# Kernel tuning notes

Measured on AMD Instinct MI355X. Metric: run time of the kernel, lower is better.

The kernel has to match this reference:

```python
import jax, jax.numpy as jnp
import numpy as np

K = 4          # conv kernel size
DIL = 3        # conv dilation
EPS = 1e-5     # rms eps inside gate kernel
NORM_EPS = 1e-5  # RMSNorm eps for value rms


def setup_inputs() -> dict:
    key = jax.random.key(0)
    ks = jax.random.split(key, 10)
    B, T, G, C, E = 2, 4096, 4, 1024, 1024
    return {
        "embeddings": jax.random.normal(ks[0], (B, T, E), jnp.float32),
        "hidden_states": jax.random.normal(ks[1], (B, T, G, C), jnp.float32),
        "key_w": jax.random.normal(ks[2], (G * C, E), jnp.float32) * 0.02,
        "key_b": jax.random.normal(ks[3], (G * C,), jnp.float32) * 0.02,
        "value_w": jax.random.normal(ks[4], (C, E), jnp.float32) * 0.02,
        "value_b": jax.random.normal(ks[5], (C,), jnp.float32) * 0.02,
        "w_key_norm": jax.random.uniform(ks[6], (G, C), jnp.float32, 0.5, 1.5),
        "w_query_norm": jax.random.uniform(ks[7], (G, C), jnp.float32, 0.5, 1.5),
        "w_norm": jax.random.uniform(ks[8], (G, C), jnp.float32, 0.5, 1.5),
        "conv_weight": jax.random.normal(ks[9], (G * C, K), jnp.float32) * 0.1,
    }


def reference(embeddings, hidden_states, key_w, key_b, value_w, value_b,
              w_key_norm, w_query_norm, w_norm, conv_weight):
    B, T, G, C = hidden_states.shape
    # projections
    k_all = (embeddings @ key_w.T + key_b).reshape(B, T, G, C)     # [B,T,G,C]
    q_all = hidden_states                                          # [B,T,G,C]
    vproj = embeddings @ value_w.T + value_b                       # [B,T,C]

    # gate kernel: per (b,t,g) RMS of key/query + weighted dot -> sign-sqrt-sigmoid gate
    rms_k = jnp.sqrt(jnp.mean(k_all * k_all, axis=-1) + EPS)       # [B,T,G]
    rms_q = jnp.sqrt(jnp.mean(q_all * q_all, axis=-1) + EPS)       # [B,T,G]
    dot = jnp.einsum('btgc,gc,btgc,gc->btg', k_all, w_key_norm, q_all, w_query_norm)
    gate_raw = dot / (rms_k * rms_q) / jnp.sqrt(jnp.float32(C))
    gate = jax.nn.sigmoid(jnp.where(gate_raw >= 0, 1.0, -1.0)
                          * jnp.sqrt(jnp.maximum(jnp.abs(gate_raw), 1e-6)))
    value = vproj[:, :, None, :] * gate[..., None]                 # [B,T,G,C]
    rms_v = jnp.sqrt(jnp.mean(value * value, axis=-1) + NORM_EPS)  # [B,T,G]

    # conv+residual kernel: per-group RMS-norm, dilated depthwise causal conv, SiLU, residual
    normed = value * (w_norm[None, None] / rms_v[..., None])       # [B,T,G,C]
    conv_w = conv_weight.reshape(G, C, K)                          # depthwise weights
    pad = (K - 1) * DIL
    xp = jnp.pad(normed, ((0, 0), (pad, 0), (0, 0), (0, 0)))
    # acc[b,t,g,c] = sum_k normed[b, t-(K-1-k)*DIL, g, c] * conv_w[g,c,k]
    acc = xp[:, 0:T] * conv_w[None, None, :, :, 0]
    for k in range(1, K):
        acc = acc + xp[:, k * DIL: k * DIL + T] * conv_w[None, None, :, :, k]
    acc = acc * jax.nn.sigmoid(acc)  # SiLU activation
    return value + acc
```

## Files before the change

kernel.cpp:

```cpp
#include <hip/hip_runtime.h>
#include <hip/hip_bf16.h>
#include <cstdint>
#include <cstddef>

using bf16 = __hip_bfloat16;

typedef __bf16 bf16x8_t __attribute__((ext_vector_type(8)));
typedef float  f32x4_t  __attribute__((ext_vector_type(4)));

static constexpr int Bb = 2;
static constexpr int Tt = 4096;
static constexpr int Gg = 4;
static constexpr int Cc = 1024;
static constexpr int Mm = Bb * Tt;
static constexpr int GC = Gg * Cc;

__device__ __forceinline__ float bfbits2f(unsigned u) {
  union { unsigned i; float f; } c; c.i = u << 16; return c.f;
}
__device__ __forceinline__ ushort f2bfbits(float v) {
  union { __hip_bfloat16 h; ushort u; } c; c.h = __float2bfloat16(v); return c.u;
}

__device__ __forceinline__ void store_val(bf16* p, float v)  { *p = __float2bfloat16(v); }
__device__ __forceinline__ void store_val(float* p, float v) { *p = v; }

__device__ __forceinline__ void gld_lds16(const ushort* g, ushort* l) {
  __builtin_amdgcn_global_load_lds(
      (const __attribute__((address_space(1))) void*)g,
      (__attribute__((address_space(3))) void*)l, 16, 0, 0);
}

__global__ __launch_bounds__(256)
void cvt_bf16(const float* __restrict__ in, ushort* __restrict__ out, int n4)
{
  const int i = blockIdx.x * 256 + threadIdx.x;
  if (i >= n4) return;
  const float4 v = ((const float4*)in)[i];
  ushort4 o;
  o.x = f2bfbits(v.x); o.y = f2bfbits(v.y);
  o.z = f2bfbits(v.z); o.w = f2bfbits(v.w);
  ((ushort4*)out)[i] = o;
}

__global__ __launch_bounds__(256)
void cvt_split(const float* __restrict__ in, ushort* __restrict__ hi,
               ushort* __restrict__ lo, int n4)
{
  const int i = blockIdx.x * 256 + threadIdx.x;
  if (i >= n4) return;
  const float4 v = ((const float4*)in)[i];
  ushort4 h, l;
  h.x = f2bfbits(v.x); l.x = f2bfbits(v.x - bfbits2f(h.x));
  h.y = f2bfbits(v.y); l.y = f2bfbits(v.y - bfbits2f(h.y));
  h.z = f2bfbits(v.z); l.z = f2bfbits(v.z - bfbits2f(h.z));
  h.w = f2bfbits(v.w); l.w = f2bfbits(v.w - bfbits2f(h.w));
  ((ushort4*)hi)[i] = h;
  ((ushort4*)lo)[i] = l;
}

__global__ __launch_bounds__(256, 2)
void gemm_key_fused(const ushort* __restrict__ embH, const ushort* __restrict__ embL,
                    const ushort* __restrict__ kwH,  const ushort* __restrict__ kwL,
                    const float* __restrict__ key_b, const float* __restrict__ hid,
                    const float* __restrict__ wkn,   const float* __restrict__ wqn,
                    float* __restrict__ k2_part, float* __restrict__ dot_part,
                    float* __restrict__ q2_part)
{
  constexpr int K = Cc;
  __shared__ __align__(16) ushort sAH[128 * 64];
  __shared__ __align__(16) ushort sAL[128 * 64];
  __shared__ __align__(16) ushort sBH[128 * 64];
  __shared__ __align__(16) ushort sBL[128 * 64];

  const int tid  = threadIdx.x;
  const int lane = tid & 63;
  const int wave = tid >> 6;
  const int wm   = wave & 1;
  const int wn   = wave >> 1;
  const int row0 = blockIdx.y * 128;
  const int col0 = blockIdx.x * 128;

  const int srow = tid >> 3;
  const int scol = ((tid & 7) ^ (srow & 7)) * 8;
  const int wofs = wave * 512;

  f32x4_t acc[4][4] = {};

  for (int kt = 0; kt < K; kt += 64) {
#pragma unroll
    for (int p = 0; p < 4; ++p) {
      const size_t aoff = (size_t)(row0 + p * 32 + srow) * K + kt + scol;
      const size_t boff = (size_t)(col0 + p * 32 + srow) * K + kt + scol;
      gld_lds16(embH + aoff, sAH + p * 2048 + wofs);
      gld_lds16(embL + aoff, sAL + p * 2048 + wofs);
      gld_lds16(kwH  + boff, sBH + p * 2048 + wofs);
      gld_lds16(kwL  + boff, sBL + p * 2048 + wofs);
    }
    __syncthreads();

#pragma unroll
    for (int ks = 0; ks < 2; ++ks) {
      const int cb = ks * 4 + (lane >> 4);
      const int ce = ((cb ^ (lane & 7)) * 8);
      bf16x8_t afH[4], afL[4], bfH[4], bfL[4];
#pragma unroll
      for (int mi = 0; mi < 4; ++mi) {
        const int r = wm * 64 + mi * 16 + (lane & 15);
        afH[mi] = *(const bf16x8_t*)(sAH + r * 64 + ce);
        afL[mi] = *(const bf16x8_t*)(sAL + r * 64 + ce);
      }
#pragma unroll
      for (int ni = 0; ni < 4; ++ni) {
        const int r = wn * 64 + ni * 16 + (lane & 15);
        bfH[ni] = *(const bf16x8_t*)(sBH + r * 64 + ce);
        bfL[ni] = *(const bf16x8_t*)(sBL + r * 64 + ce);
      }
#pragma unroll
      for (int mi = 0; mi < 4; ++mi)
#pragma unroll
        for (int ni = 0; ni < 4; ++ni) {
          acc[mi][ni] = __builtin_amdgcn_mfma_f32_16x16x32_bf16(
              afH[mi], bfH[ni], acc[mi][ni], 0, 0, 0);
          acc[mi][ni] = __builtin_amdgcn_mfma_f32_16x16x32_bf16(
              afH[mi], bfL[ni], acc[mi][ni], 0, 0, 0);
          acc[mi][ni] = __builtin_amdgcn_mfma_f32_16x16x32_bf16(
              afL[mi], bfH[ni], acc[mi][ni], 0, 0, 0);
        }
    }
    __syncthreads();
  }

  const int lrow = lane >> 4;
  const int lcol = lane & 15;
  const int g    = col0 >> 10;

  float s2[4][4] = {};
  float su[4][4] = {};
  float sq[4][4] = {};

#pragma unroll
  for (int ni = 0; ni < 4; ++ni) {
    const int col = col0 + wn * 64 + ni * 16 + lcol;
    const float kb = key_b[col];
    const float ww = wkn[col] * wqn[col];
#pragma unroll
    for (int mi = 0; mi < 4; ++mi) {
      const int rowb = row0 + wm * 64 + mi * 16 + lrow * 4;
#pragma unroll
      for (int r = 0; r < 4; ++r) {
        const float q = hid[(size_t)(rowb + r) * GC + col];
        const float k = acc[mi][ni][r] + kb;
        s2[mi][r] += k * k;
        su[mi][r] += k * ww * q;
        sq[mi][r] += q * q;
      }
    }
  }
#pragma unroll
  for (int off = 1; off < 16; off <<= 1) {
#pragma unroll
    for (int mi = 0; mi < 4; ++mi)
#pragma unroll
      for (int r = 0; r < 4; ++r) {
        s2[mi][r] += __shfl_xor(s2[mi][r], off);
        su[mi][r] += __shfl_xor(su[mi][r], off);
        sq[mi][r] += __shfl_xor(sq[mi][r], off);
      }
  }
  if (lcol == 0) {
#pragma unroll
    for (int mi = 0; mi < 4; ++mi) {
      const int rowb = row0 + wm * 64 + mi * 16 + lrow * 4;
#pragma unroll
      for (int r = 0; r < 4; ++r) {
        atomicAdd(&k2_part[(rowb + r) * Gg + g],  s2[mi][r]);
        atomicAdd(&dot_part[(rowb + r) * Gg + g], su[mi][r]);
        atomicAdd(&q2_part[(rowb + r) * Gg + g],  sq[mi][r]);
      }
    }
  }
}

template <typename OutT>
__global__ __launch_bounds__(256, 2)
void gemm_bt(const ushort* __restrict__ A, const ushort* __restrict__ Bm,
             const float* __restrict__ bias, OutT* __restrict__ C,
             int M, int N, int K)
{
  __shared__ __align__(16) ushort sA[128 * 64];
  __shared__ __align__(16) ushort sB[128 * 64];

  const int tid  = threadIdx.x;
  const int lane = tid & 63;
  const int wave = tid >> 6;
  const int wm   = wave & 1;
  const int wn   = wave >> 1;
  const int row0 = blockIdx.y * 128;
  const int col0 = blockIdx.x * 128;

  const int srow = tid >> 3;
  const int scol = ((tid & 7) ^ (srow & 7)) * 8;
  ushort* aWB = sA + wave * 512;
  ushort* bWB = sB + wave * 512;

  f32x4_t acc[4][4] = {};

  for (int kt = 0; kt < K; kt += 64) {
#pragma unroll
    for (int p = 0; p < 4; ++p) {
      gld_lds16(A  + (size_t)(row0 + p * 32 + srow) * K + kt + scol,
                aWB + p * 2048);
      gld_lds16(Bm + (size_t)(col0 + p * 32 + srow) * K + kt + scol,
                bWB + p * 2048);
    }
    __syncthreads();

#pragma unroll
    for (int ks = 0; ks < 2; ++ks) {
      const int cb = ks * 4 + (lane >> 4);
      const int ce = ((cb ^ (lane & 7)) * 8);
      bf16x8_t af[4], bfr[4];
#pragma unroll
      for (int mi = 0; mi < 4; ++mi) {
        const int r = wm * 64 + mi * 16 + (lane & 15);
        af[mi] = *(const bf16x8_t*)(sA + r * 64 + ce);
      }
#pragma unroll
      for (int ni = 0; ni < 4; ++ni) {
        const int r = wn * 64 + ni * 16 + (lane & 15);
        bfr[ni] = *(const bf16x8_t*)(sB + r * 64 + ce);
      }
#pragma unroll
      for (int mi = 0; mi < 4; ++mi)
#pragma unroll
        for (int ni = 0; ni < 4; ++ni)
          acc[mi][ni] = __builtin_amdgcn_mfma_f32_16x16x32_bf16(
              af[mi], bfr[ni], acc[mi][ni], 0, 0, 0);
    }
    __syncthreads();
  }

  const int lrow = lane >> 4;
  const int lcol = lane & 15;
#pragma unroll
  for (int ni = 0; ni < 4; ++ni) {
    const int col = col0 + wn * 64 + ni * 16 + lcol;
    const float bv = bias[col];
#pragma unroll
    for (int mi = 0; mi < 4; ++mi) {
      const int rowb = row0 + wm * 64 + mi * 16 + lrow * 4;
#pragma unroll
      for (int r = 0; r < 4; ++r)
        store_val(&C[(size_t)(rowb + r) * N + col], acc[mi][ni][r] + bv);
    }
  }
}

__global__ __launch_bounds__(256)
void finalize_kernel(const float* __restrict__ vproj,
                     const float* __restrict__ k2_part,
                     const float* __restrict__ dot_part,
                     const float* __restrict__ q2_part,
                     float* __restrict__ gate_o, float* __restrict__ snorm_o)
{
  const int bt   = blockIdx.x;
  const int tid  = threadIdx.x;
  const int g    = tid >> 6;
  const int lane = tid & 63;

  const float4 v4 = ((const float4*)(vproj + (size_t)bt * Cc))[tid];
  float pv = v4.x * v4.x + v4.y * v4.y + v4.z * v4.z + v4.w * v4.w;
#pragma unroll
  for (int off = 32; off > 0; off >>= 1) pv += __shfl_xor(pv, off);
  __shared__ float wsum[4];
  if (lane == 0) wsum[g] = pv;
  __syncthreads();

  if (lane == 0) {
    const float mv = (wsum[0] + wsum[1] + wsum[2] + wsum[3]) * (1.0f / 1024.0f);
    const float sk = k2_part[bt * Gg + g];
    const float sd = dot_part[bt * Gg + g];
    const float sq = q2_part[bt * Gg + g];
    const float rk = sqrtf(sk * (1.0f / 1024.0f) + 1e-5f);
    const float rq = sqrtf(sq * (1.0f / 1024.0f) + 1e-5f);
    const float graw = sd / (rk * rq) * (1.0f / 32.0f);
    const float sgn = (graw >= 0.f) ? 1.f : -1.f;
    const float gate = 1.f / (1.f + expf(-sgn * sqrtf(fmaxf(fabsf(graw), 1e-6f))));
    const float rv = sqrtf(gate * gate * mv + 1e-5f);
    gate_o[bt * Gg + g]  = gate;
    snorm_o[bt * Gg + g] = gate / rv;
  }
}

static constexpr int CJ  = 128;
static constexpr int NCH = 11;

__global__ __launch_bounds__(256)
void conv_kernel(const float* __restrict__ vproj, const float* __restrict__ gate,
                 const float* __restrict__ snorm, const float* __restrict__ wnm,
                 const float* __restrict__ cw, float* __restrict__ out)
{
  int x = blockIdx.x;
  const int cb = x & 3;  x >>= 2;
  const int p  = x % 3;  x /= 3;
  const int ch = x % NCH; x /= NCH;
  const int g  = x & 3;  x >>= 2;
  const int b  = x;
  const int c  = cb * 256 + threadIdx.x;

  const float wn = wnm[g * Cc + c];
  const float4 w = ((const float4*)cw)[g * Cc + c];

  int t = p + 3 * (ch * CJ);
  if (t >= Tt) return;

  float n1 = 0.f, n2 = 0.f, n3 = 0.f;
#pragma unroll
  for (int h = 3; h >= 1; --h) {
    const int th = t - 3 * h;
    float nv = 0.f;
    if (th >= 0) {
      const int bt = b * Tt + th;
      nv = vproj[(size_t)bt * Cc + c] * snorm[bt * Gg + g] * wn;
    }
    n3 = n2; n2 = n1; n1 = nv;
  }

  for (int j = 0; j < CJ && t < Tt; ++j, t += 3) {
    const int bt = b * Tt + t;
    const float vp  = vproj[(size_t)bt * Cc + c];
    const float gt  = gate[bt * Gg + g];
    const float sn  = snorm[bt * Gg + g];
    const float cur = vp * sn * wn;
    const float a   = w.x * n3 + w.y * n2 + w.z * n1 + w.w * cur;
    const float si  = a / (1.f + __expf(-a));
    out[((size_t)bt * Gg + g) * Cc + c] = vp * gt + si;
    n3 = n2; n2 = n1; n1 = cur;
  }
}

extern "C" void kernel_launch(void* const* d_in, const int* in_sizes, int n_in,
                              void* d_out, int out_size, void* d_ws, size_t ws_size,
                              hipStream_t stream)
{
  const float* emb   = (const float*)d_in[0];
  const float* hid   = (const float*)d_in[1];
  const float* key_w = (const float*)d_in[2];
  const float* key_b = (const float*)d_in[3];
  const float* val_w = (const float*)d_in[4];
  const float* val_b = (const float*)d_in[5];
  const float* wkn   = (const float*)d_in[6];
  const float* wqn   = (const float*)d_in[7];
  const float* wnm   = (const float*)d_in[8];
  const float* cwt   = (const float*)d_in[9];
  float* out = (float*)d_out;

  char* ws = (char*)d_ws;
  ushort* embH  = (ushort*)ws;  ws += (size_t)Mm * Cc * 2;
  ushort* embL  = (ushort*)ws;  ws += (size_t)Mm * Cc * 2;
  ushort* kwH   = (ushort*)ws;  ws += (size_t)GC * Cc * 2;
  ushort* kwL   = (ushort*)ws;  ws += (size_t)GC * Cc * 2;
  ushort* vwB   = (ushort*)ws;  ws += (size_t)Cc * Cc * 2;
  float*  vproj = (float*)ws;   ws += (size_t)Mm * Cc * 4;
  float*  k2p   = (float*)ws;   ws += (size_t)Mm * Gg * 4;
  float*  dotp  = (float*)ws;   ws += (size_t)Mm * Gg * 4;
  float*  q2p   = (float*)ws;   ws += (size_t)Mm * Gg * 4;
  float*  gate  = (float*)ws;   ws += (size_t)Mm * Gg * 4;
  float*  snorm = (float*)ws;

  hipMemsetAsync(k2p, 0, (size_t)3 * Mm * Gg * 4, stream);

  dim3 blk(256);
  cvt_split<<<dim3((Mm * Cc / 4) / 256), blk, 0, stream>>>(emb,   embH, embL, Mm * Cc / 4);
  cvt_split<<<dim3((GC * Cc / 4) / 256), blk, 0, stream>>>(key_w, kwH,  kwL,  GC * Cc / 4);
  cvt_bf16 <<<dim3((Cc * Cc / 4) / 256), blk, 0, stream>>>(val_w, vwB,  Cc * Cc / 4);

  gemm_key_fused<<<dim3(GC / 128, Mm / 128), blk, 0, stream>>>(
      embH, embL, kwH, kwL, key_b, hid, wkn, wqn, k2p, dotp, q2p);

  gemm_bt<float><<<dim3(Cc / 128, Mm / 128), blk, 0, stream>>>(
      embH, vwB, val_b, vproj, Mm, Cc, Cc);

  finalize_kernel<<<dim3(Mm), blk, 0, stream>>>(vproj, k2p, dotp, q2p, gate, snorm);

  const int nblocks = Bb * Gg * NCH * 3 * (Cc / 256);
  conv_kernel<<<dim3(nblocks), blk, 0, stream>>>(vproj, gate, snorm, wnm, cwt, out);
}
```

Before: 600.6 us.

## Double-buffer LDS tiles in both GEMM kernels to overlap loads with MFMA

Both the fused key GEMM and the generic bf16 GEMM now use two LDS buffers and prefetch the next K-tile with direct global-to-LDS loads while the current tile feeds the MFMAs. Explicit vmcnt waits and raw barriers replace __syncthreads. The split-bf16 key kernel also shrinks its K-tile from 64 to 32 with a new XOR swizzle, so the LDS footprint stays the same as before. The aim is to hide global memory latency behind compute, at the cost of more barriers per K step in the key kernel and reliance on hand-counted vmcnt values.

```diff
diff --git a/kernel.cpp b/kernel.cpp
--- a/kernel.cpp
+++ b/kernel.cpp
@@ -67,11 +67,12 @@
                     float* __restrict__ k2_part, float* __restrict__ dot_part,
                     float* __restrict__ q2_part)
 {
-  constexpr int K = Cc;
-  __shared__ __align__(16) ushort sAH[128 * 64];
-  __shared__ __align__(16) ushort sAL[128 * 64];
-  __shared__ __align__(16) ushort sBH[128 * 64];
-  __shared__ __align__(16) ushort sBL[128 * 64];
+  constexpr int K  = Cc;
+  constexpr int NT = K / 32;
+  __shared__ __align__(16) ushort sAH[2 * 4096];
+  __shared__ __align__(16) ushort sAL[2 * 4096];
+  __shared__ __align__(16) ushort sBH[2 * 4096];
+  __shared__ __align__(16) ushort sBL[2 * 4096];
 
   const int tid  = threadIdx.x;
   const int lane = tid & 63;
@@ -81,54 +82,81 @@
   const int row0 = blockIdx.y * 128;
   const int col0 = blockIdx.x * 128;
 
-  const int srow = tid >> 3;
-  const int scol = ((tid & 7) ^ (srow & 7)) * 8;
+  const int sr0 = tid >> 2;
+  const int sch = tid & 3;
   const int wofs = wave * 512;
 
+  int gcol[2]; int grA[2];
+#pragma unroll
+  for (int p = 0; p < 2; ++p) {
+    const int r = p * 64 + sr0;
+    gcol[p] = ((sch ^ ((r + (r >> 2)) & 3)) * 8);
+    grA[p]  = r;
+  }
+
   f32x4_t acc[4][4] = {};
 
-  for (int kt = 0; kt < K; kt += 64) {
-#pragma unroll
-    for (int p = 0; p < 4; ++p) {
-      const size_t aoff = (size_t)(row0 + p * 32 + srow) * K + kt + scol;
-      const size_t boff = (size_t)(col0 + p * 32 + srow) * K + kt + scol;
-      gld_lds16(embH + aoff, sAH + p * 2048 + wofs);
-      gld_lds16(embL + aoff, sAL + p * 2048 + wofs);
-      gld_lds16(kwH  + boff, sBH + p * 2048 + wofs);
-      gld_lds16(kwL  + boff, sBL + p * 2048 + wofs);
-    }
-    __syncthreads();
-
-#pragma unroll
-    for (int ks = 0; ks < 2; ++ks) {
-      const int cb = ks * 4 + (lane >> 4);
-      const int ce = ((cb ^ (lane & 7)) * 8);
-      bf16x8_t afH[4], afL[4], bfH[4], bfL[4];
-#pragma unroll
-      for (int mi = 0; mi < 4; ++mi) {
-        const int r = wm * 64 + mi * 16 + (lane & 15);
-        afH[mi] = *(const bf16x8_t*)(sAH + r * 64 + ce);
-        afL[mi] = *(const bf16x8_t*)(sAL + r * 64 + ce);
-      }
+  auto stage = [&](int kt, int b) {
+    const int kk = kt * 32;
+#pragma unroll
+    for (int p = 0; p < 2; ++p) {
+      const size_t ao = (size_t)(row0 + grA[p]) * K + kk + gcol[p];
+      const size_t bo = (size_t)(col0 + grA[p]) * K + kk + gcol[p];
+      const int d = b * 4096 + p * 2048 + wofs;
+      gld_lds16(embH + ao, sAH + d);
+      gld_lds16(embL + ao, sAL + d);
+      gld_lds16(kwH  + bo, sBH + d);
+      gld_lds16(kwL  + bo, sBL + d);
+    }
+  };
+
+  stage(0, 0);
+  int cur = 0;
+
+  for (int kt = 0; kt < NT; ++kt) {
+    if (kt + 1 < NT) {
+      stage(kt + 1, cur ^ 1);
+      asm volatile("s_waitcnt vmcnt(8)" ::: "memory");
+    } else {
+      asm volatile("s_waitcnt vmcnt(0)" ::: "memory");
+    }
+    asm volatile("s_barrier" ::: "memory");
+
+    const ushort* bAH = sAH + cur * 4096;
+    const ushort* bAL = sAL + cur * 4096;
+    const ushort* bBH = sBH + cur * 4096;
+    const ushort* bBL = sBL + cur * 4096;
+    const int ch = lane >> 4;
+
+    bf16x8_t afH[4], afL[4], bfH[4], bfL[4];
+#pragma unroll
+    for (int mi = 0; mi < 4; ++mi) {
+      const int r  = wm * 64 + mi * 16 + (lane & 15);
+      const int co = ((ch ^ ((r + (r >> 2)) & 3)) * 8);
+      afH[mi] = *(const bf16x8_t*)(bAH + r * 32 + co);
+      afL[mi] = *(const bf16x8_t*)(bAL + r * 32 + co);
+    }
+#pragma unroll
+    for (int ni = 0; ni < 4; ++ni) {
+      const int r  = wn * 64 + ni * 16 + (lane & 15);
+      const int co = ((ch ^ ((r + (r >> 2)) & 3)) * 8);
+      bfH[ni] = *(const bf16x8_t*)(bBH + r * 32 + co);
+      bfL[ni] = *(const bf16x8_t*)(bBL + r * 32 + co);
+    }
+#pragma unroll
+    for (int mi = 0; mi < 4; ++mi)
 #pragma unroll
       for (int ni = 0; ni < 4; ++ni) {
-        const int r = wn * 64 + ni * 16 + (lane & 15);
-        bfH[ni] = *(const bf16x8_t*)(sBH + r * 64 + ce);
-        bfL[ni] = *(const bf16x8_t*)(sBL + r * 64 + ce);
-      }
-#pragma unroll
-      for (int mi = 0; mi < 4; ++mi)
-#pragma unroll
-        for (int ni = 0; ni < 4; ++ni) {
-          acc[mi][ni] = __builtin_amdgcn_mfma_f32_16x16x32_bf16(
-              afH[mi], bfH[ni], acc[mi][ni], 0, 0, 0);
-          acc[mi][ni] = __builtin_amdgcn_mfma_f32_16x16x32_bf16(
-              afH[mi], bfL[ni], acc[mi][ni], 0, 0, 0);
-          acc[mi][ni] = __builtin_amdgcn_mfma_f32_16x16x32_bf16(
-              afL[mi], bfH[ni], acc[mi][ni], 0, 0, 0);
-        }
-    }
-    __syncthreads();
+        acc[mi][ni] = __builtin_amdgcn_mfma_f32_16x16x32_bf16(
+            afH[mi], bfH[ni], acc[mi][ni], 0, 0, 0);
+        acc[mi][ni] = __builtin_amdgcn_mfma_f32_16x16x32_bf16(
+            afH[mi], bfL[ni], acc[mi][ni], 0, 0, 0);
+        acc[mi][ni] = __builtin_amdgcn_mfma_f32_16x16x32_bf16(
+            afL[mi], bfH[ni], acc[mi][ni], 0, 0, 0);
+      }
+
+    asm volatile("s_barrier" ::: "memory");
+    cur ^= 1;
   }
 
   const int lrow = lane >> 4;
@@ -188,8 +216,8 @@
              const float* __restrict__ bias, OutT* __restrict__ C,
              int M, int N, int K)
 {
-  __shared__ __align__(16) ushort sA[128 * 64];
-  __shared__ __align__(16) ushort sB[128 * 64];
+  __shared__ __align__(16) ushort sA[2 * 128 * 64];
+  __shared__ __align__(16) ushort sB[2 * 128 * 64];
 
   const int tid  = threadIdx.x;
   const int lane = tid & 63;
@@ -201,20 +229,36 @@
 
   const int srow = tid >> 3;
   const int scol = ((tid & 7) ^ (srow & 7)) * 8;
-  ushort* aWB = sA + wave * 512;
-  ushort* bWB = sB + wave * 512;
+  const int wofs = wave * 512;
 
   f32x4_t acc[4][4] = {};
 
-  for (int kt = 0; kt < K; kt += 64) {
+  const int NT = K / 64;
+
+  auto stage = [&](int kt, int b) {
+    const int kk = kt * 64;
 #pragma unroll
     for (int p = 0; p < 4; ++p) {
-      gld_lds16(A  + (size_t)(row0 + p * 32 + srow) * K + kt + scol,
-                aWB + p * 2048);
-      gld_lds16(Bm + (size_t)(col0 + p * 32 + srow) * K + kt + scol,
-                bWB + p * 2048);
-    }
-    __syncthreads();
+      const int d = b * 8192 + p * 2048 + wofs;
+      gld_lds16(A  + (size_t)(row0 + p * 32 + srow) * K + kk + scol, sA + d);
+      gld_lds16(Bm + (size_t)(col0 + p * 32 + srow) * K + kk + scol, sB + d);
+    }
+  };
+
+  stage(0, 0);
+  int cur = 0;
+
+  for (int kt = 0; kt < NT; ++kt) {
+    if (kt + 1 < NT) {
+      stage(kt + 1, cur ^ 1);
+      asm volatile("s_waitcnt vmcnt(8)" ::: "memory");
+    } else {
+      asm volatile("s_waitcnt vmcnt(0)" ::: "memory");
+    }
+    asm volatile("s_barrier" ::: "memory");
+
+    const ushort* bA = sA + cur * 8192;
+    const ushort* bB = sB + cur * 8192;
 
 #pragma unroll
     for (int ks = 0; ks < 2; ++ks) {
@@ -224,12 +268,12 @@
 #pragma unroll
       for (int mi = 0; mi < 4; ++mi) {
         const int r = wm * 64 + mi * 16 + (lane & 15);
-        af[mi] = *(const bf16x8_t*)(sA + r * 64 + ce);
+        af[mi] = *(const bf16x8_t*)(bA + r * 64 + ce);
       }
 #pragma unroll
       for (int ni = 0; ni < 4; ++ni) {
         const int r = wn * 64 + ni * 16 + (lane & 15);
-        bfr[ni] = *(const bf16x8_t*)(sB + r * 64 + ce);
+        bfr[ni] = *(const bf16x8_t*)(bB + r * 64 + ce);
       }
 #pragma unroll
       for (int mi = 0; mi < 4; ++mi)
@@ -238,7 +282,9 @@
           acc[mi][ni] = __builtin_amdgcn_mfma_f32_16x16x32_bf16(
               af[mi], bfr[ni], acc[mi][ni], 0, 0, 0);
     }
-    __syncthreads();
+
+    asm volatile("s_barrier" ::: "memory");
+    cur ^= 1;
   }
 
   const int lrow = lane >> 4;
```

Measured after the change: 633.4 us. 5.5% more time.

## Halve key GEMM LDS footprint by interleaving hi/lo in one tile, raise occupancy

Applied to the files above, without the earlier changes.

The fused key GEMM now packs the hi and lo bf16 halves of each 32-wide K slice into a single 64-column swizzled LDS tile per operand, which halves its shared memory use from 64KB to 32KB. The K step drops from 64 to 32, so there are twice as many iterations and barriers. Launch bounds for both GEMM kernels go from 2 to 4 blocks per SM, which may force register limits and spills given the 16 accumulator fragments. The goal is more resident waves to hide global-to-LDS latency, at the cost of more sync overhead per unit of work.

```diff
diff --git a/kernel.cpp b/kernel.cpp
--- a/kernel.cpp
+++ b/kernel.cpp
@@ -59,7 +59,7 @@
   ((ushort4*)lo)[i] = l;
 }
 
-__global__ __launch_bounds__(256, 2)
+__global__ __launch_bounds__(256, 4)
 void gemm_key_fused(const ushort* __restrict__ embH, const ushort* __restrict__ embL,
                     const ushort* __restrict__ kwH,  const ushort* __restrict__ kwL,
                     const float* __restrict__ key_b, const float* __restrict__ hid,
@@ -68,10 +68,8 @@
                     float* __restrict__ q2_part)
 {
   constexpr int K = Cc;
-  __shared__ __align__(16) ushort sAH[128 * 64];
-  __shared__ __align__(16) ushort sAL[128 * 64];
-  __shared__ __align__(16) ushort sBH[128 * 64];
-  __shared__ __align__(16) ushort sBL[128 * 64];
+  __shared__ __align__(16) ushort sA[128 * 64];
+  __shared__ __align__(16) ushort sB[128 * 64];
 
   const int tid  = threadIdx.x;
   const int lane = tid & 63;
@@ -82,52 +80,51 @@
   const int col0 = blockIdx.x * 128;
 
   const int srow = tid >> 3;
-  const int scol = ((tid & 7) ^ (srow & 7)) * 8;
-  const int wofs = wave * 512;
+  const int schk = (tid & 7) ^ (srow & 7);
+  const ushort* aBase = (schk < 4) ? embH : embL;
+  const ushort* bBase = (schk < 4) ? kwH  : kwL;
+  const int selem = (schk & 3) * 8;
+  const int wofs  = wave * 512;
 
   f32x4_t acc[4][4] = {};
 
-  for (int kt = 0; kt < K; kt += 64) {
+  for (int kt = 0; kt < K; kt += 32) {
 #pragma unroll
     for (int p = 0; p < 4; ++p) {
-      const size_t aoff = (size_t)(row0 + p * 32 + srow) * K + kt + scol;
-      const size_t boff = (size_t)(col0 + p * 32 + srow) * K + kt + scol;
-      gld_lds16(embH + aoff, sAH + p * 2048 + wofs);
-      gld_lds16(embL + aoff, sAL + p * 2048 + wofs);
-      gld_lds16(kwH  + boff, sBH + p * 2048 + wofs);
-      gld_lds16(kwL  + boff, sBL + p * 2048 + wofs);
+      gld_lds16(aBase + (size_t)(row0 + p * 32 + srow) * K + kt + selem,
+                sA + p * 2048 + wofs);
+      gld_lds16(bBase + (size_t)(col0 + p * 32 + srow) * K + kt + selem,
+                sB + p * 2048 + wofs);
     }
     __syncthreads();
 
-#pragma unroll
-    for (int ks = 0; ks < 2; ++ks) {
-      const int cb = ks * 4 + (lane >> 4);
-      const int ce = ((cb ^ (lane & 7)) * 8);
-      bf16x8_t afH[4], afL[4], bfH[4], bfL[4];
-#pragma unroll
-      for (int mi = 0; mi < 4; ++mi) {
-        const int r = wm * 64 + mi * 16 + (lane & 15);
-        afH[mi] = *(const bf16x8_t*)(sAH + r * 64 + ce);
-        afL[mi] = *(const bf16x8_t*)(sAL + r * 64 + ce);
-      }
+    const int cH = (lane >> 4) ^ (lane & 7);
+    const int cL = cH ^ 4;
+
+    bf16x8_t afH[4], afL[4], bfH[4], bfL[4];
+#pragma unroll
+    for (int mi = 0; mi < 4; ++mi) {
+      const int r = wm * 64 + mi * 16 + (lane & 15);
+      afH[mi] = *(const bf16x8_t*)(sA + r * 64 + cH * 8);
+      afL[mi] = *(const bf16x8_t*)(sA + r * 64 + cL * 8);
+    }
+#pragma unroll
+    for (int ni = 0; ni < 4; ++ni) {
+      const int r = wn * 64 + ni * 16 + (lane & 15);
+      bfH[ni] = *(const bf16x8_t*)(sB + r * 64 + cH * 8);
+      bfL[ni] = *(const bf16x8_t*)(sB + r * 64 + cL * 8);
+    }
+#pragma unroll
+    for (int mi = 0; mi < 4; ++mi)
 #pragma unroll
       for (int ni = 0; ni < 4; ++ni) {
-        const int r = wn * 64 + ni * 16 + (lane & 15);
-        bfH[ni] = *(const bf16x8_t*)(sBH + r * 64 + ce);
-        bfL[ni] = *(const bf16x8_t*)(sBL + r * 64 + ce);
-      }
-#pragma unroll
-      for (int mi = 0; mi < 4; ++mi)
-#pragma unroll
-        for (int ni = 0; ni < 4; ++ni) {
-          acc[mi][ni] = __builtin_amdgcn_mfma_f32_16x16x32_bf16(
-              afH[mi], bfH[ni], acc[mi][ni], 0, 0, 0);
-          acc[mi][ni] = __builtin_amdgcn_mfma_f32_16x16x32_bf16(
-              afH[mi], bfL[ni], acc[mi][ni], 0, 0, 0);
-          acc[mi][ni] = __builtin_amdgcn_mfma_f32_16x16x32_bf16(
-              afL[mi], bfH[ni], acc[mi][ni], 0, 0, 0);
-        }
-    }
+        acc[mi][ni] = __builtin_amdgcn_mfma_f32_16x16x32_bf16(
+            afH[mi], bfH[ni], acc[mi][ni], 0, 0, 0);
+        acc[mi][ni] = __builtin_amdgcn_mfma_f32_16x16x32_bf16(
+            afH[mi], bfL[ni], acc[mi][ni], 0, 0, 0);
+        acc[mi][ni] = __builtin_amdgcn_mfma_f32_16x16x32_bf16(
+            afL[mi], bfH[ni], acc[mi][ni], 0, 0, 0);
+      }
     __syncthreads();
   }
 
@@ -183,7 +180,7 @@
 }
 
 template <typename OutT>
-__global__ __launch_bounds__(256, 2)
+__global__ __launch_bounds__(256, 4)
 void gemm_bt(const ushort* __restrict__ A, const ushort* __restrict__ Bm,
              const float* __restrict__ bias, OutT* __restrict__ C,
              int M, int N, int K)
```

Measured after the change: 615.5 us. +2.5%, slower.
